# Kernel optimization log

Measured on AMD Instinct MI355X. Metric: run time of the kernel, lower is better.

The kernel has to match this reference:

```python
import jax, jax.numpy as jnp
import numpy as np

N, E, F, C, H, O, ED = 100000, 1600000, 64, 64, 1, 32, 16
M = 20000  # number of masked (selected) nodes


def gat_layer(x, src, dst, edge_attr, W, a_s, a_d, We, a_e, b, n, h, c):
    # x: [n, in], W: [in, h*c], a_*: [h, c], We: [ed, h*c], b: [h*c]
    hx = (x @ W).reshape(n, h, c)                       # node features per head
    alpha_s = (hx * a_s).sum(-1)                        # [n, h]
    alpha_d = (hx * a_d).sum(-1)                        # [n, h]
    he = (edge_attr @ We).reshape(-1, h, c)             # [e, h, c]
    alpha = alpha_s[src] + alpha_d[dst] + (he * a_e).sum(-1)  # [e, h]
    alpha = jax.nn.leaky_relu(alpha, 0.2)
    # segment softmax over incoming edges of each destination node
    mx = jax.ops.segment_max(alpha, dst, num_segments=n)
    ex = jnp.exp(alpha - mx[dst])
    denom = jax.ops.segment_sum(ex, dst, num_segments=n)
    coef = ex / denom[dst]                              # [e, h]
    out = jax.ops.segment_sum(coef[:, :, None] * hx[src], dst, num_segments=n)
    return out.reshape(n, h * c) + b


def setup_inputs() -> dict:
    key = jax.random.key(0)
    ks = jax.random.split(key, 16)
    s = 0.1
    inp = {
        "x": jax.random.normal(ks[0], (N, F), jnp.float32),
        "edge_index": jax.random.randint(ks[1], (2, E), 0, N, jnp.int32),
        "mask": jax.random.randint(ks[2], (M,), 0, N, jnp.int32),
        "edge_attr": jax.random.normal(ks[3], (E, ED), jnp.float32),
        # conv1 params
        "W1": jax.random.normal(ks[4], (F, H * C), jnp.float32) * s,
        "a_s1": jax.random.normal(ks[5], (H, C), jnp.float32) * s,
        "a_d1": jax.random.normal(ks[6], (H, C), jnp.float32) * s,
        "We1": jax.random.normal(ks[7], (ED, H * C), jnp.float32) * s,
        "a_e1": jax.random.normal(ks[8], (H, C), jnp.float32) * s,
        "b1": jnp.zeros((H * C,), jnp.float32),
        # conv2 params
        "W2": jax.random.normal(ks[9], (H * C, H * O), jnp.float32) * s,
        "a_s2": jax.random.normal(ks[10], (H, O), jnp.float32) * s,
        "a_d2": jax.random.normal(ks[11], (H, O), jnp.float32) * s,
        "We2": jax.random.normal(ks[12], (ED, H * O), jnp.float32) * s,
        "a_e2": jax.random.normal(ks[13], (H, O), jnp.float32) * s,
        "b2": jnp.zeros((H * O,), jnp.float32),
    }
    return inp


def reference(x, edge_index, mask, edge_attr,
              W1, a_s1, a_d1, We1, a_e1, b1,
              W2, a_s2, a_d2, We2, a_e2, b2):
    # add self loops with fill_value=0 edge attributes (GATConv fill_value=0)
    loops = jnp.arange(N, dtype=edge_index.dtype)
    src = jnp.concatenate([edge_index[0], loops])
    dst = jnp.concatenate([edge_index[1], loops])
    ea = jnp.concatenate([edge_attr, jnp.zeros((N, ED), edge_attr.dtype)], axis=0)

    h1 = jax.nn.elu(gat_layer(x, src, dst, ea, W1, a_s1, a_d1, We1, a_e1, b1, N, H, C))
    h2 = jax.nn.elu(gat_layer(h1, src, dst, ea, W2, a_s2, a_d2, We2, a_e2, b2, N, H, O))
    return h2[mask]  # [M, O]; squeeze() is a no-op here
```

## Files before the change

### kernel.cpp

```cpp
#include <hip/hip_runtime.h>
#include <hip/hip_bf16.h>
#include <hip/hip_fp16.h>
#include <math.h>

#define NN 100000
#define EE 1600000
#define MM 20000
#define EPB 768
#define NBLK ((EE + EPB - 1) / EPB)
#define NBC 250
#define BWC 400
#define N_SCAN (NBC * NBLK + 1)
#define SMASK 0x1FFFF

__global__ void k_v(const float* __restrict__ We1, const float* __restrict__ ae1v,
                    const float* __restrict__ We2, const float* __restrict__ ae2v,
                    float* __restrict__ v1, float* __restrict__ v2) {
    int t = threadIdx.x;
    if (t < 16) {
        float s = 0.f;
        for (int c = 0; c < 64; ++c) s += We1[t * 64 + c] * ae1v[c];
        v1[t] = s;
    } else if (t < 32) {
        int r = t - 16;
        float s = 0.f;
        for (int c = 0; c < 32; ++c) s += We2[r * 32 + c] * ae2v[c];
        v2[r] = s;
    }
}

__global__ __launch_bounds__(256) void k_node1(
    const float* __restrict__ x, const float* __restrict__ W,
    const float* __restrict__ a_s, const float* __restrict__ a_d,
    __half* __restrict__ hx, float* __restrict__ aS, float* __restrict__ aD,
    int n_nodes)
{
    __shared__ float Wl[64 * 64];
    __shared__ float xs[4][64];
    int tid = threadIdx.x;
#pragma unroll
    for (int i = 0; i < 16; ++i) Wl[tid + i * 256] = W[tid + i * 256];
    int wv = tid >> 6, lane = tid & 63;
    int n = blockIdx.x * 4 + wv;
    bool act = (n < n_nodes);
    if (act) xs[wv][lane] = x[(size_t)n * 64 + lane];
    __syncthreads();
    if (!act) return;
    float h = 0.f;
#pragma unroll
    for (int k = 0; k < 64; ++k) h += xs[wv][k] * Wl[k * 64 + lane];
    hx[(size_t)n * 64 + lane] = __float2half(h);
    float ps = h * a_s[lane];
    float pd = h * a_d[lane];
#pragma unroll
    for (int o = 32; o > 0; o >>= 1) { ps += __shfl_xor(ps, o); pd += __shfl_xor(pd, o); }
    if (lane == 0) { aS[n] = ps; aD[n] = pd; }
}

__global__ __launch_bounds__(256) void k_aebh(
    const float* __restrict__ ea, const float* __restrict__ v1, const float* __restrict__ v2,
    const int* __restrict__ dst, unsigned* __restrict__ ae12,
    int* __restrict__ bh, int E)
{
    __shared__ int hl[NBC];
    int tid = threadIdx.x, blk = blockIdx.x;
    for (int j = tid; j < NBC; j += 256) hl[j] = 0;
    __syncthreads();
    const float4* v14 = (const float4*)v1;
    const float4* v24 = (const float4*)v2;
    float4 va0 = v14[0], va1 = v14[1], va2 = v14[2], va3 = v14[3];
    float4 vb0 = v24[0], vb1 = v24[1], vb2 = v24[2], vb3 = v24[3];
    int e0 = blk * EPB, e1 = min(E, e0 + EPB);
    for (int e = e0 + tid; e < e1; e += 256) {
        const float4* p4 = (const float4*)(ea + (size_t)e * 16);
        float4 q0 = p4[0], q1 = p4[1], q2 = p4[2], q3 = p4[3];
        float s1 = q0.x * va0.x + q0.y * va0.y + q0.z * va0.z + q0.w * va0.w
                 + q1.x * va1.x + q1.y * va1.y + q1.z * va1.z + q1.w * va1.w
                 + q2.x * va2.x + q2.y * va2.y + q2.z * va2.z + q2.w * va2.w
                 + q3.x * va3.x + q3.y * va3.y + q3.z * va3.z + q3.w * va3.w;
        float s2 = q0.x * vb0.x + q0.y * vb0.y + q0.z * vb0.z + q0.w * vb0.w
                 + q1.x * vb1.x + q1.y * vb1.y + q1.z * vb1.z + q1.w * vb1.w
                 + q2.x * vb2.x + q2.y * vb2.y + q2.z * vb2.z + q2.w * vb2.w
                 + q3.x * vb3.x + q3.y * vb3.y + q3.z * vb3.z + q3.w * vb3.w;
        ae12[e] = (unsigned)__half_as_ushort(__float2half(s1))
                | ((unsigned)__half_as_ushort(__float2half(s2)) << 16);
        atomicAdd(&hl[dst[e] / BWC], 1);
    }
    __syncthreads();
    for (int j = tid; j < NBC; j += 256) bh[j * NBLK + blk] = hl[j];
    if (blk == 0 && tid == 0) bh[NBC * NBLK] = 0;
}

__global__ __launch_bounds__(256) void k_scan1(const int* __restrict__ deg, int* __restrict__ pre,
                                               int* __restrict__ bsum, int n) {
    __shared__ int wsum[4];
    int t = threadIdx.x;
    int base = blockIdx.x * 2048 + t * 8;
    int v[8]; int s = 0;
#pragma unroll
    for (int i = 0; i < 8; ++i) { int idx = base + i; int d = (idx < n) ? deg[idx] : 0; v[i] = s; s += d; }
    int lane = t & 63, wv = t >> 6;
    int incl = s;
#pragma unroll
    for (int off = 1; off < 64; off <<= 1) { int y = __shfl_up(incl, off); if (lane >= off) incl += y; }
    if (lane == 63) wsum[wv] = incl;
    __syncthreads();
    int woff = 0;
    for (int w = 0; w < wv; ++w) woff += wsum[w];
    int texcl = woff + incl - s;
#pragma unroll
    for (int i = 0; i < 8; ++i) { int idx = base + i; if (idx < n) pre[idx] = texcl + v[i]; }
    if (t == 255) bsum[blockIdx.x] = woff + incl;
}

__global__ __launch_bounds__(256) void k_scan2(int* __restrict__ bsum, int nb) {
    __shared__ int ws[4];
    int t = threadIdx.x, lane = t & 63, wv = t >> 6;
    int x = (t < nb) ? bsum[t] : 0;
    int incl = x;
#pragma unroll
    for (int off = 1; off < 64; off <<= 1) { int y = __shfl_up(incl, off); if (lane >= off) incl += y; }
    if (lane == 63) ws[wv] = incl;
    __syncthreads();
    int woff = 0;
    for (int w = 0; w < wv; ++w) woff += ws[w];
    if (t < nb) bsum[t] = woff + incl - x;
}

__global__ void k_scan3b(int* __restrict__ pre, const int* __restrict__ bsum, int n) {
    int i = blockIdx.x * 256 + threadIdx.x;
    if (i < n) pre[i] += bsum[i >> 11];
}

__global__ __launch_bounds__(256) void k_part(
    const int* __restrict__ src, const int* __restrict__ dst,
    const unsigned* __restrict__ ae12,
    const int* __restrict__ scanned, uint2* __restrict__ recMid, int E)
{
    __shared__ int lcur[NBC];
    int tid = threadIdx.x, blk = blockIdx.x;
    for (int j = tid; j < NBC; j += 256) lcur[j] = scanned[j * NBLK + blk];
    __syncthreads();
    int e0 = blk * EPB, e1 = min(E, e0 + EPB);
    for (int e = e0 + tid; e < e1; e += 256) {
        int s = src[e], d = dst[e];
        unsigned w = ae12[e];
        int b = d / BWC;
        int dloc = d - b * BWC;
        unsigned lo = (unsigned)s | ((unsigned)dloc << 17);
        int pos = atomicAdd(&lcur[b], 1);
        recMid[pos] = make_uint2(lo, w);
    }
}

__global__ __launch_bounds__(256) void k_build(
    const int* __restrict__ scanned, const uint2* __restrict__ recMid,
    int* __restrict__ rowptr, uint2* __restrict__ rec, int E)
{
    __shared__ int hist[BWC];
    __shared__ int lofs[BWC];
    __shared__ int wsum[4];
    int tid = threadIdx.x, b = blockIdx.x;
    int B0 = scanned[b * NBLK];
    int B1 = scanned[(b + 1) * NBLK];
    for (int j = tid; j < BWC; j += 256) hist[j] = 0;
    __syncthreads();
    for (int i = B0 + tid; i < B1; i += 256) atomicAdd(&hist[recMid[i].x >> 17], 1);
    __syncthreads();
    int lane = tid & 63, wv = tid >> 6;
    int i0 = 2 * tid, i1 = 2 * tid + 1;
    int a0 = (i0 < BWC) ? hist[i0] : 0;
    int a1 = (i1 < BWC) ? hist[i1] : 0;
    int s = a0 + a1;
    int incl = s;
#pragma unroll
    for (int off = 1; off < 64; off <<= 1) { int y = __shfl_up(incl, off); if (lane >= off) incl += y; }
    if (lane == 63) wsum[wv] = incl;
    __syncthreads();
    int woff = 0;
    for (int w = 0; w < wv; ++w) woff += wsum[w];
    int base = woff + incl - s;
    if (i0 < BWC) lofs[i0] = base;
    if (i1 < BWC) lofs[i1] = base + a0;
    __syncthreads();
    for (int j = tid; j < BWC; j += 256) rowptr[b * BWC + j] = B0 + lofs[j];
    if (b == NBC - 1 && tid == 0) rowptr[NN] = E;
    __syncthreads();
    for (int i = B0 + tid; i < B1; i += 256) {
        uint2 r = recMid[i];
        int nl = (int)(r.x >> 17);
        int p = atomicAdd(&lofs[nl], 1);
        rec[B0 + p] = r;
    }
}

__global__ __launch_bounds__(256) void k_agg1(
    const int* __restrict__ rowptr,
    const uint2* __restrict__ rec, const __half* __restrict__ hx,
    const float* __restrict__ aS, const float* __restrict__ aD,
    const float* __restrict__ b, float* __restrict__ h1, int n_nodes)
{
    int wv = threadIdx.x >> 6, lane = threadIdx.x & 63;
    int n = blockIdx.x * 4 + wv;
    if (n >= n_nodes) return;
    int start = rowptr[n], end = rowptr[n + 1];
    float aDn = aD[n];
    float r = 0.f, den = 0.f;
    for (int base = start; base < end; base += 64) {
        int cnt = min(end - base, 64);
        int s = 0; float ex = 0.f;
        if (lane < cnt) {
            uint2 R = rec[base + lane];
            s = (int)(R.x & SMASK);
            float s1 = __half2float(__ushort_as_half((unsigned short)(R.y & 0xFFFFu)));
            float a = aS[s] + aDn + s1;
            a = a > 0.f ? a : 0.2f * a;
            ex = __expf(a);
        }
        int j = 0;
        for (; j + 4 <= cnt; j += 4) {
            int s0 = __shfl(s, j), s1i = __shfl(s, j + 1), s2 = __shfl(s, j + 2), s3 = __shfl(s, j + 3);
            float e0 = __shfl(ex, j), e1 = __shfl(ex, j + 1), e2 = __shfl(ex, j + 2), e3 = __shfl(ex, j + 3);
            float h0 = __half2float(hx[(size_t)s0 * 64 + lane]);
            float h1v = __half2float(hx[(size_t)s1i * 64 + lane]);
            float h2 = __half2float(hx[(size_t)s2 * 64 + lane]);
            float h3 = __half2float(hx[(size_t)s3 * 64 + lane]);
            r += e0 * h0; r += e1 * h1v; r += e2 * h2; r += e3 * h3;
            den += e0 + e1 + e2 + e3;
        }
        for (; j < cnt; ++j) {
            int sj = __shfl(s, j); float ej = __shfl(ex, j);
            r += ej * __half2float(hx[(size_t)sj * 64 + lane]);
            den += ej;
        }
    }
    float al = aS[n] + aDn;
    al = al > 0.f ? al : 0.2f * al;
    float exl = __expf(al);
    float hself = __half2float(hx[(size_t)n * 64 + lane]);
    float val = (r + exl * hself) / (den + exl) + b[lane];
    h1[(size_t)n * 64 + lane] = val > 0.f ? val : expm1f(val);
}

__global__ __launch_bounds__(256) void k_node2(
    const float* __restrict__ h1, const float* __restrict__ W,
    const float* __restrict__ a_s, const float* __restrict__ a_d,
    float* __restrict__ hx, float* __restrict__ aS, float* __restrict__ aD, int n_nodes)
{
    __shared__ float Wl[64 * 32];
    __shared__ float xs[8][64];
    int tid = threadIdx.x;
#pragma unroll
    for (int i = 0; i < 8; ++i) Wl[tid + i * 256] = W[tid + i * 256];
    int n0 = blockIdx.x * 8;
    for (int i = tid; i < 8 * 64; i += 256) {
        int r = i >> 6;
        int n = n0 + r;
        xs[r][i & 63] = (n < n_nodes) ? h1[(size_t)n * 64 + (i & 63)] : 0.f;
    }
    __syncthreads();
    int g = tid >> 5, c = tid & 31;
    int n = n0 + g;
    if (n >= n_nodes) return;
    float h = 0.f;
#pragma unroll
    for (int k = 0; k < 64; ++k) h += xs[g][k] * Wl[k * 32 + c];
    hx[(size_t)n * 32 + c] = h;
    float ps = h * a_s[c], pd = h * a_d[c];
#pragma unroll
    for (int o = 16; o > 0; o >>= 1) { ps += __shfl_xor(ps, o, 32); pd += __shfl_xor(pd, o, 32); }
    if (c == 0) { aS[n] = ps; aD[n] = pd; }
}

__global__ __launch_bounds__(256) void k_agg2(
    const int* __restrict__ mask, const int* __restrict__ rowptr,
    const uint2* __restrict__ rec, const float* __restrict__ hx,
    const float* __restrict__ aS, const float* __restrict__ aD,
    const float* __restrict__ b, float* __restrict__ out, int m_cnt)
{
    int wv = threadIdx.x >> 6, lane = threadIdx.x & 63;
    int m = blockIdx.x * 4 + wv;
    if (m >= m_cnt) return;
    int n = mask[m];
    int start = rowptr[n], end = rowptr[n + 1];
    float aDn = aD[n];
    int half = lane >> 5, c = lane & 31;
    float r = 0.f, den = 0.f;
    for (int base = start; base < end; base += 64) {
        int cnt = min(end - base, 64);
        int s = 0; float ex = 0.f;
        if (lane < cnt) {
            uint2 R = rec[base + lane];
            s = (int)(R.x & SMASK);
            float ae2 = __half2float(__ushort_as_half((unsigned short)(R.y >> 16)));
            float a = aS[s] + aDn + ae2;
            a = a > 0.f ? a : 0.2f * a;
            ex = __expf(a);
        }
        int j = 0;
        for (; j + 8 <= cnt; j += 8) {
            int j0 = j + half, j2 = j + 2 + half, j4 = j + 4 + half, j6 = j + 6 + half;
            int s0 = __shfl(s, j0), s2v = __shfl(s, j2), s4 = __shfl(s, j4), s6 = __shfl(s, j6);
            float e0 = __shfl(ex, j0), e2 = __shfl(ex, j2), e4 = __shfl(ex, j4), e6 = __shfl(ex, j6);
            r += e0 * hx[(size_t)s0 * 32 + c];
            r += e2 * hx[(size_t)s2v * 32 + c];
            r += e4 * hx[(size_t)s4 * 32 + c];
            r += e6 * hx[(size_t)s6 * 32 + c];
            den += e0 + e2 + e4 + e6;
        }
        for (; j < cnt; j += 2) {
            int jj = j + half;
            if (jj < cnt) {
                int sj = __shfl(s, jj); float ej = __shfl(ex, jj);
                r += ej * hx[(size_t)sj * 32 + c];
                den += ej;
            }
        }
    }
    float ro = __shfl(r, lane ^ 32);
    float do_ = __shfl(den, lane ^ 32);
    r += ro; den += do_;
    if (half == 0) {
        float al = aS[n] + aDn;
        al = al > 0.f ? al : 0.2f * al;
        float exl = __expf(al);
        float val = (r + exl * hx[(size_t)n * 32 + c]) / (den + exl) + b[c];
        out[(size_t)m * 32 + c] = val > 0.f ? val : expm1f(val);
    }
}

extern "C" void kernel_launch(void* const* d_in, const int* in_sizes, int n_in,
                              void* d_out, int out_size, void* d_ws, size_t ws_size,
                              hipStream_t stream) {
    const float* x    = (const float*)d_in[0];
    const int*   ei   = (const int*)d_in[1];
    const int*   mask = (const int*)d_in[2];
    const float* ea   = (const float*)d_in[3];
    const float* W1   = (const float*)d_in[4];
    const float* a_s1 = (const float*)d_in[5];
    const float* a_d1 = (const float*)d_in[6];
    const float* We1  = (const float*)d_in[7];
    const float* a_e1 = (const float*)d_in[8];
    const float* b1   = (const float*)d_in[9];
    const float* W2   = (const float*)d_in[10];
    const float* a_s2 = (const float*)d_in[11];
    const float* a_d2 = (const float*)d_in[12];
    const float* We2  = (const float*)d_in[13];
    const float* a_e2 = (const float*)d_in[14];
    const float* b2   = (const float*)d_in[15];
    const int* src = ei;
    const int* dst = ei + EE;
    float* out = (float*)d_out;

    char* w = (char*)d_ws;
    size_t off = 0;
    auto take = [&](size_t bytes) -> char* {
        char* p = w + off;
        off += (bytes + 255) & ~(size_t)255;
        return p;
    };
    float*    v1      = (float*)take(16 * 4);
    float*    v2      = (float*)take(16 * 4);
    __half*   hx1h    = (__half*)take((size_t)NN * 64 * 2);
    float*    aS1     = (float*)take((size_t)NN * 4);
    float*    aD1     = (float*)take((size_t)NN * 4);
    float*    h1      = (float*)take((size_t)NN * 64 * 4);
    float*    hx2     = (float*)take((size_t)NN * 32 * 4);
    float*    aS2     = (float*)take((size_t)NN * 4);
    float*    aD2     = (float*)take((size_t)NN * 4);
    int*      rowptr  = (int*)take(((size_t)NN + 1) * 4);
    unsigned* ae12    = (unsigned*)take((size_t)EE * 4);
    int*      bh      = (int*)take((size_t)N_SCAN * 4);
    int*      scanned = (int*)take((size_t)N_SCAN * 4);
    int*      bsum    = (int*)take(256 * 4);
    uint2*    recMid  = (uint2*)take((size_t)EE * 8);
    uint2*    rec     = (uint2*)take((size_t)EE * 8);

    const int nb_bh = (N_SCAN + 2047) / 2048;

    k_v<<<1, 64, 0, stream>>>(We1, a_e1, We2, a_e2, v1, v2);
    k_node1<<<(NN + 3) / 4, 256, 0, stream>>>(x, W1, a_s1, a_d1, hx1h, aS1, aD1, NN);
    k_aebh<<<NBLK, 256, 0, stream>>>(ea, v1, v2, dst, ae12, bh, EE);
    k_scan1<<<nb_bh, 256, 0, stream>>>(bh, scanned, bsum, N_SCAN);
    k_scan2<<<1, 256, 0, stream>>>(bsum, nb_bh);
    k_scan3b<<<(N_SCAN + 255) / 256, 256, 0, stream>>>(scanned, bsum, N_SCAN);
    k_part<<<NBLK, 256, 0, stream>>>(src, dst, ae12, scanned, recMid, EE);
    k_build<<<NBC, 256, 0, stream>>>(scanned, recMid, rowptr, rec, EE);
    k_agg1<<<(NN + 3) / 4, 256, 0, stream>>>(rowptr, rec, hx1h, aS1, aD1, b1, h1, NN);
    k_node2<<<(NN + 7) / 8, 256, 0, stream>>>(h1, W2, a_s2, a_d2, hx2, aS2, aD2, NN);
    k_agg2<<<(MM + 3) / 4, 256, 0, stream>>>(mask, rowptr, rec, hx2, aS2, aD2, b2, out, MM);
}
```

Before: 240.3 us.

## Hold node-transform weights in registers with persistent waves and shuffles

Both node projection kernels now keep the weight column in registers per lane and run as a fixed grid of persistent waves that loop over nodes. Each step broadcasts input features with wave shuffles instead of staging them through shared memory. This removes the per-block reload of W into LDS and the block barriers. The cost is much higher register pressure (64 floats per lane) and 64 shuffles per node, which may lower occupancy.

```diff
diff --git a/kernel.cpp b/kernel.cpp
--- a/kernel.cpp
+++ b/kernel.cpp
@@ -35,26 +35,24 @@
     __half* __restrict__ hx, float* __restrict__ aS, float* __restrict__ aD,
     int n_nodes)
 {
-    __shared__ float Wl[64 * 64];
-    __shared__ float xs[4][64];
-    int tid = threadIdx.x;
-#pragma unroll
-    for (int i = 0; i < 16; ++i) Wl[tid + i * 256] = W[tid + i * 256];
-    int wv = tid >> 6, lane = tid & 63;
-    int n = blockIdx.x * 4 + wv;
-    bool act = (n < n_nodes);
-    if (act) xs[wv][lane] = x[(size_t)n * 64 + lane];
-    __syncthreads();
-    if (!act) return;
-    float h = 0.f;
-#pragma unroll
-    for (int k = 0; k < 64; ++k) h += xs[wv][k] * Wl[k * 64 + lane];
-    hx[(size_t)n * 64 + lane] = __float2half(h);
-    float ps = h * a_s[lane];
-    float pd = h * a_d[lane];
-#pragma unroll
-    for (int o = 32; o > 0; o >>= 1) { ps += __shfl_xor(ps, o); pd += __shfl_xor(pd, o); }
-    if (lane == 0) { aS[n] = ps; aD[n] = pd; }
+    int lane = threadIdx.x & 63;
+    int wid = (blockIdx.x * 256 + threadIdx.x) >> 6;
+    int nwaves = gridDim.x * 4;
+    float wreg[64];
+#pragma unroll
+    for (int k = 0; k < 64; ++k) wreg[k] = W[k * 64 + lane];
+    float as = a_s[lane], ad = a_d[lane];
+    for (int n = wid; n < n_nodes; n += nwaves) {
+        float xr = x[(size_t)n * 64 + lane];
+        float h = 0.f;
+#pragma unroll
+        for (int k = 0; k < 64; ++k) h += __shfl(xr, k) * wreg[k];
+        hx[(size_t)n * 64 + lane] = __float2half(h);
+        float ps = h * as, pd = h * ad;
+#pragma unroll
+        for (int o = 32; o > 0; o >>= 1) { ps += __shfl_xor(ps, o); pd += __shfl_xor(pd, o); }
+        if (lane == 0) { aS[n] = ps; aD[n] = pd; }
+    }
 }
 
 __global__ __launch_bounds__(256) void k_aebh(
@@ -247,29 +245,38 @@
     const float* __restrict__ a_s, const float* __restrict__ a_d,
     float* __restrict__ hx, float* __restrict__ aS, float* __restrict__ aD, int n_nodes)
 {
-    __shared__ float Wl[64 * 32];
-    __shared__ float xs[8][64];
-    int tid = threadIdx.x;
-#pragma unroll
-    for (int i = 0; i < 8; ++i) Wl[tid + i * 256] = W[tid + i * 256];
-    int n0 = blockIdx.x * 8;
-    for (int i = tid; i < 8 * 64; i += 256) {
-        int r = i >> 6;
-        int n = n0 + r;
-        xs[r][i & 63] = (n < n_nodes) ? h1[(size_t)n * 64 + (i & 63)] : 0.f;
-    }
-    __syncthreads();
-    int g = tid >> 5, c = tid & 31;
-    int n = n0 + g;
-    if (n >= n_nodes) return;
-    float h = 0.f;
-#pragma unroll
-    for (int k = 0; k < 64; ++k) h += xs[g][k] * Wl[k * 32 + c];
-    hx[(size_t)n * 32 + c] = h;
-    float ps = h * a_s[c], pd = h * a_d[c];
-#pragma unroll
-    for (int o = 16; o > 0; o >>= 1) { ps += __shfl_xor(ps, o, 32); pd += __shfl_xor(pd, o, 32); }
-    if (c == 0) { aS[n] = ps; aD[n] = pd; }
+    int lane = threadIdx.x & 63;
+    int half = lane >> 5, c = lane & 31;
+    int wid = (blockIdx.x * 256 + threadIdx.x) >> 6;
+    int nwaves = gridDim.x * 4;
+    float wreg[64];
+#pragma unroll
+    for (int k = 0; k < 64; ++k) wreg[k] = W[k * 32 + c];
+    float as = a_s[c], ad = a_d[c];
+    int npairs = (n_nodes + 1) >> 1;
+    for (int p = wid; p < npairs; p += nwaves) {
+        int n = p * 2 + half;
+        bool act = (n < n_nodes);
+        float xr0 = 0.f, xr1 = 0.f;
+        if (act) {
+            xr0 = h1[(size_t)n * 64 + c];
+            xr1 = h1[(size_t)n * 64 + 32 + c];
+        }
+        float h = 0.f;
+        int base = half << 5;
+#pragma unroll
+        for (int k = 0; k < 32; ++k) {
+            h += __shfl(xr0, base + k) * wreg[k];
+            h += __shfl(xr1, base + k) * wreg[32 + k];
+        }
+        if (act) {
+            hx[(size_t)n * 32 + c] = h;
+            float ps = h * as, pd = h * ad;
+#pragma unroll
+            for (int o = 16; o > 0; o >>= 1) { ps += __shfl_xor(ps, o, 32); pd += __shfl_xor(pd, o, 32); }
+            if (c == 0) { aS[n] = ps; aD[n] = pd; }
+        }
+    }
 }
 
 __global__ __launch_bounds__(256) void k_agg2(
@@ -379,7 +386,7 @@
     const int nb_bh = (N_SCAN + 2047) / 2048;
 
     k_v<<<1, 64, 0, stream>>>(We1, a_e1, We2, a_e2, v1, v2);
-    k_node1<<<(NN + 3) / 4, 256, 0, stream>>>(x, W1, a_s1, a_d1, hx1h, aS1, aD1, NN);
+    k_node1<<<1024, 256, 0, stream>>>(x, W1, a_s1, a_d1, hx1h, aS1, aD1, NN);
     k_aebh<<<NBLK, 256, 0, stream>>>(ea, v1, v2, dst, ae12, bh, EE);
     k_scan1<<<nb_bh, 256, 0, stream>>>(bh, scanned, bsum, N_SCAN);
     k_scan2<<<1, 256, 0, stream>>>(bsum, nb_bh);
@@ -387,6 +394,6 @@
     k_part<<<NBLK, 256, 0, stream>>>(src, dst, ae12, scanned, recMid, EE);
     k_build<<<NBC, 256, 0, stream>>>(scanned, recMid, rowptr, rec, EE);
     k_agg1<<<(NN + 3) / 4, 256, 0, stream>>>(rowptr, rec, hx1h, aS1, aD1, b1, h1, NN);
-    k_node2<<<(NN + 7) / 8, 256, 0, stream>>>(h1, W2, a_s2, a_d2, hx2, aS2, aD2, NN);
+    k_node2<<<1024, 256, 0, stream>>>(h1, W2, a_s2, a_d2, hx2, aS2, aD2, NN);
     k_agg2<<<(MM + 3) / 4, 256, 0, stream>>>(mask, rowptr, rec, hx2, aS2, aD2, b2, out, MM);
 }
```

Result: slower. 280.9 us (+16.9%).
